# Performance work log

Measured on AMD Instinct MI355X. Metric: run time of the kernel, lower is better.

The kernel has to match this reference:

```python
import jax, jax.numpy as jnp
import numpy as np
import itertools

B, H, W, C = 64, 28, 28, 576
NH, WS = 18, 7
KD = C // NH          # head dim = 32 (attn_ratio=1 so d == key_dim)
HID = 4 * C           # mlp hidden
N = WS * WS           # tokens per window = 49


def _bias_idxs():
    points = list(itertools.product(range(WS), range(WS)))
    offsets, idxs = {}, []
    for p1 in points:
        for p2 in points:
            off = (abs(p1[0] - p2[0]), abs(p1[1] - p2[1]))
            if off not in offsets:
                offsets[off] = len(offsets)
            idxs.append(offsets[off])
    return np.asarray(idxs, dtype=np.int64).reshape(N, N), len(offsets)


def setup_inputs() -> dict:
    key = jax.random.key(0)
    ks = jax.random.split(key, 10)
    idxs, n_off = _bias_idxs()  # n_off == 49
    s = 0.02
    return {
        "x": jax.random.normal(ks[0], (B, H * W, C), jnp.float32),
        "gamma_a": jnp.ones((C,), jnp.float32),
        "beta_a": jnp.zeros((C,), jnp.float32),
        "qkv_w": jax.random.normal(ks[1], (3 * C, C), jnp.float32) * s,
        "qkv_b": jnp.zeros((3 * C,), jnp.float32),
        "proj_w": jax.random.normal(ks[2], (C, C), jnp.float32) * s,
        "proj_b": jnp.zeros((C,), jnp.float32),
        "attn_biases": jax.random.normal(ks[3], (NH, n_off), jnp.float32) * s,
        "conv_w": jax.random.normal(ks[4], (C, 1, 3, 3), jnp.float32) * 0.1,
        "bn_gamma": jnp.ones((C,), jnp.float32),
        "bn_beta": jnp.zeros((C,), jnp.float32),
        "bn_mean": jnp.zeros((C,), jnp.float32),
        "bn_var": jax.random.uniform(ks[5], (C,), jnp.float32, 0.5, 1.5),
        "gamma_m": jnp.ones((C,), jnp.float32),
        "beta_m": jnp.zeros((C,), jnp.float32),
        "fc1_w": jax.random.normal(ks[6], (HID, C), jnp.float32) * s,
        "fc1_b": jnp.zeros((HID,), jnp.float32),
        "fc2_w": jax.random.normal(ks[7], (C, HID), jnp.float32) * s,
        "fc2_b": jnp.zeros((C,), jnp.float32),
        "bias_idxs": jnp.asarray(idxs),
    }


def _ln(x, g, b, eps=1e-5):
    mu = x.mean(-1, keepdims=True)
    var = ((x - mu) ** 2).mean(-1, keepdims=True)
    return (x - mu) * jax.lax.rsqrt(var + eps) * g + b


def reference(x, gamma_a, beta_a, qkv_w, qkv_b, proj_w, proj_b, attn_biases,
              conv_w, bn_gamma, bn_beta, bn_mean, bn_var,
              gamma_m, beta_m, fc1_w, fc1_b, fc2_w, fc2_b, bias_idxs):
    scale = KD ** -0.5
    nWh, nWw = H // WS, W // WS
    res = x
    # ---- window partition: (B, H*W, C) -> (B*nWh*nWw, 49, C) ----
    xw = x.reshape(B, nWh, WS, nWw, WS, C).transpose(0, 1, 3, 2, 4, 5)
    xw = xw.reshape(-1, N, C)
    # ---- windowed attention with gathered relative-position bias ----
    h = _ln(xw, gamma_a, beta_a)
    qkv = h @ qkv_w.T + qkv_b                       # (Bw, N, 3C)
    qkv = qkv.reshape(-1, N, NH, 3 * KD)
    q, k, v = jnp.split(qkv, 3, axis=-1)            # each (Bw, N, NH, KD)
    q = q.transpose(0, 2, 1, 3)
    k = k.transpose(0, 2, 1, 3)
    v = v.transpose(0, 2, 1, 3)
    bias = attn_biases[:, bias_idxs]                # (NH, N, N)
    attn = jnp.einsum('bhnd,bhmd->bhnm', q, k) * scale + bias
    attn = jax.nn.softmax(attn, axis=-1)
    out = jnp.einsum('bhnm,bhmd->bhnd', attn, v)    # (Bw, NH, N, KD)
    out = out.transpose(0, 2, 1, 3).reshape(-1, N, C) @ proj_w.T + proj_b
    # ---- window reverse ----
    out = out.reshape(B, nWh, nWw, WS, WS, C).transpose(0, 1, 3, 2, 4, 5)
    out = out.reshape(B, H * W, C)
    x = res + out
    # ---- depthwise 3x3 conv + BatchNorm (inference stats) ----
    xc = x.transpose(0, 2, 1).reshape(B, C, H, W)
    xc = jax.lax.conv_general_dilated(
        xc, conv_w, (1, 1), [(1, 1), (1, 1)],
        feature_group_count=C,
        dimension_numbers=('NCHW', 'OIHW', 'NCHW'))
    eps = 1e-5
    inv = (jax.lax.rsqrt(bn_var + eps) * bn_gamma)[:, None, None]
    xc = (xc - bn_mean[:, None, None]) * inv + bn_beta[:, None, None]
    x = xc.reshape(B, C, H * W).transpose(0, 2, 1)
    # ---- MLP with pre-LayerNorm ----
    hm = _ln(x, gamma_m, beta_m)
    hm = jax.nn.gelu(hm @ fc1_w.T + fc1_b, approximate=False)
    hm = hm @ fc2_w.T + fc2_b
    return x + hm
```

## Files before the change

kernel.cpp:

```cpp
#include <hip/hip_runtime.h>
#include <hip/hip_bf16.h>

typedef __bf16 v8bf  __attribute__((ext_vector_type(8)));
typedef __bf16 v4bf  __attribute__((ext_vector_type(4)));
typedef float  f32x4 __attribute__((ext_vector_type(4)));
typedef float  f32x8 __attribute__((ext_vector_type(8)));

#define TOKENS 50176
#define CDIM   576
#define NHEAD  18
#define QKVD   1728

__device__ __forceinline__ void gld16(const __bf16* g, __bf16* l)
{
    __builtin_amdgcn_global_load_lds(
        (const __attribute__((address_space(1))) void*)g,
        (__attribute__((address_space(3))) void*)l,
        16, 0, 0);
}

__device__ __forceinline__ float fast_gelu(float x)
{
    const float z  = x * 0.70710678118654752f;
    const float az = fabsf(z);
    const float t  = __frcp_rn(1.0f + 0.3275911f * az);
    float p = 1.061405429f;
    p = p * t - 1.453152027f;
    p = p * t + 1.421413741f;
    p = p * t - 0.284496736f;
    p = p * t + 0.254829592f;
    const float e   = __expf(-z * z);
    float erfv = 1.0f - p * t * e;
    erfv = copysignf(erfv, z);
    return 0.5f * x * (1.0f + erfv);
}

__global__ __launch_bounds__(256)
void cast_kernel(const float* __restrict__ in, __bf16* __restrict__ out)
{
    const size_t i = ((size_t)blockIdx.x * 256 + threadIdx.x) * 4;
    f32x4 v = *(const f32x4*)&in[i];
    v4bf o;
#pragma unroll
    for (int j = 0; j < 4; ++j) o[j] = (__bf16)v[j];
    *(v4bf*)&out[i] = o;
}

__global__ __launch_bounds__(64)
void conv_prep(const float* __restrict__ w, const float* __restrict__ bg,
               const float* __restrict__ bb, const float* __restrict__ bm,
               const float* __restrict__ bv, __bf16* __restrict__ wt,
               float* __restrict__ bias2)
{
    const int c = blockIdx.x * 64 + threadIdx.x;
    const float inv = rsqrtf(bv[c] + 1e-5f) * bg[c];
#pragma unroll
    for (int t = 0; t < 9; ++t) wt[t * CDIM + c] = (__bf16)(w[c * 9 + t] * inv);
    bias2[c] = bb[c] - bm[c] * inv;
}

__global__ __launch_bounds__(256)
void ln_kernel(const float* __restrict__ x, const float* __restrict__ g,
               const float* __restrict__ b, __bf16* __restrict__ out)
{
    const int lane = threadIdx.x & 63;
    const int wid  = threadIdx.x >> 6;
    const size_t t = (size_t)blockIdx.x * 4 + wid;
    const float* row = x + t * CDIM;

    float v[16];
    float sum = 0.f, sq = 0.f;
    {
        f32x8 d0 = *(const f32x8*)&row[(size_t)lane * 8];
#pragma unroll
        for (int j = 0; j < 8; ++j) { float f = d0[j]; v[j] = f; sum += f; sq += f * f; }
    }
    if (lane < 8) {
        f32x8 d1 = *(const f32x8*)&row[(size_t)(lane + 64) * 8];
#pragma unroll
        for (int j = 0; j < 8; ++j) { float f = d1[j]; v[8 + j] = f; sum += f; sq += f * f; }
    }
#pragma unroll
    for (int o = 32; o >= 1; o >>= 1) {
        sum += __shfl_xor(sum, o, 64);
        sq  += __shfl_xor(sq,  o, 64);
    }
    const float mean = sum * (1.0f / CDIM);
    const float rstd = rsqrtf(sq * (1.0f / CDIM) - mean * mean + 1e-5f);

    {
        int c0 = lane * 8;
        v8bf o0;
#pragma unroll
        for (int j = 0; j < 8; ++j)
            o0[j] = (__bf16)((v[j] - mean) * rstd * g[c0 + j] + b[c0 + j]);
        *(v8bf*)&out[t * CDIM + c0] = o0;
    }
    if (lane < 8) {
        int c0 = (lane + 64) * 8;
        v8bf o1;
#pragma unroll
        for (int j = 0; j < 8; ++j)
            o1[j] = (__bf16)((v[8 + j] - mean) * rstd * g[c0 + j] + b[c0 + j]);
        *(v8bf*)&out[t * CDIM + c0] = o1;
    }
}

template<int BM, int EPI, typename OutT, typename AddT>
__global__ __launch_bounds__(512, 1)
void gemm_bt(const __bf16* __restrict__ A, const __bf16* __restrict__ W,
             const float* __restrict__ bias, const AddT* __restrict__ add,
             OutT* __restrict__ C, int N, int K, int nN)
{
    constexpr int BK  = 32;
    constexpr int ASZ = BM * BK;
    constexpr int BSZ = 192 * BK;
    constexpr int MFR = BM / 32;
    constexpr int MH  = MFR / 2;
    __shared__ __bf16 L[4][ASZ + BSZ];
    const int tid = threadIdx.x, lane = tid & 63, wid = tid >> 6;
    const int lr = lane & 15, kh = lane >> 4;
    const int wm = wid >> 2, wn = wid & 3;

    const int nwg = gridDim.x, bid = blockIdx.x;
    const int q = nwg >> 3, r = nwg & 7;
    const int xcd = bid & 7, jc = bid >> 3;
    const int wgid = (xcd < r ? xcd * (q + 1) : r * (q + 1) + (xcd - r) * q) + jc;
    const int mblk = wgid / nN, nblk = wgid - mblk * nN;
    const int m0 = mblk * BM, n0 = nblk * 192;

    const __bf16* pA;
    if constexpr (BM == 256) pA = A + (size_t)(m0 + wid * 32 + lr) * K + kh * 8;
    else                     pA = A + (size_t)(m0 + wid * 16 + lr) * K + kh * 8;
    const __bf16* pW = W + (size_t)(n0 + (wid < 6 ? wid : 0) * 32 + lr) * K + kh * 8;

    auto stageA = [&](int s, int kt) {
        if constexpr (BM == 256) {
#pragma unroll
            for (int i = 0; i < 2; ++i)
                gld16(pA + (size_t)(i * 16) * K + kt * BK, &L[s][(wid * 2 + i) * 512]);
        } else {
            gld16(pA + kt * BK, &L[s][wid * 512]);
        }
    };
    auto stageB = [&](int s, int kt) {
        if (wid < 6) {
#pragma unroll
            for (int i = 0; i < 2; ++i)
                gld16(pW + (size_t)(i * 16) * K + kt * BK,
                      &L[s][ASZ + (wid * 2 + i) * 512]);
        }
    };

    const int lo = lane * 8;

    f32x4 acc[MFR][3] = {};
    const int NT = K / BK;

    stageA(0, 0); stageB(0, 0);
    stageA(1, 1); stageB(1, 1);

    for (int t = 0; t < NT; ++t) {
        if (t + 1 < NT) {
            if constexpr (BM == 256) {
                if (wid < 6) asm volatile("s_waitcnt vmcnt(4)" ::: "memory");
                else         asm volatile("s_waitcnt vmcnt(2)" ::: "memory");
            } else {
                if (wid < 6) asm volatile("s_waitcnt vmcnt(3)" ::: "memory");
                else         asm volatile("s_waitcnt vmcnt(1)" ::: "memory");
            }
        } else {
            asm volatile("s_waitcnt vmcnt(0)" ::: "memory");
        }
        __builtin_amdgcn_s_barrier();

        const __bf16* Ls = L[t & 3];
        v8bf bfr[3], afr[MH];

#pragma unroll
        for (int nf = 0; nf < 3; ++nf)
            bfr[nf] = *(const v8bf*)&Ls[ASZ + (wn * 3 + nf) * 512 + lo];
#pragma unroll
        for (int mf = 0; mf < MH; ++mf)
            afr[mf] = *(const v8bf*)&Ls[(wm * MFR + mf) * 512 + lo];

        if (t + 2 < NT) stageA((t + 2) & 3, t + 2);

        __builtin_amdgcn_s_setprio(1);
#pragma unroll
        for (int mf = 0; mf < MH; ++mf)
#pragma unroll
            for (int nf = 0; nf < 3; ++nf)
                acc[mf][nf] = __builtin_amdgcn_mfma_f32_16x16x32_bf16(
                    afr[mf], bfr[nf], acc[mf][nf], 0, 0, 0);
        __builtin_amdgcn_s_setprio(0);
        __builtin_amdgcn_s_barrier();

#pragma unroll
        for (int mf = 0; mf < MH; ++mf)
            afr[mf] = *(const v8bf*)&Ls[(wm * MFR + MH + mf) * 512 + lo];

        if (t + 2 < NT) stageB((t + 2) & 3, t + 2);

        __builtin_amdgcn_s_setprio(1);
#pragma unroll
        for (int mf = 0; mf < MH; ++mf)
#pragma unroll
            for (int nf = 0; nf < 3; ++nf)
                acc[MH + mf][nf] = __builtin_amdgcn_mfma_f32_16x16x32_bf16(
                    afr[mf], bfr[nf], acc[MH + mf][nf], 0, 0, 0);
        __builtin_amdgcn_s_setprio(0);
    }

#pragma unroll
    for (int mf = 0; mf < MFR; ++mf)
#pragma unroll
        for (int nf = 0; nf < 3; ++nf)
#pragma unroll
            for (int rr = 0; rr < 4; ++rr) {
                int row = m0 + wm * (BM / 2) + mf * 16 + kh * 4 + rr;
                int col = n0 + wn * 48 + nf * 16 + lr;
                float vv = acc[mf][nf][rr] + bias[col];
                if (EPI == 1) vv += (float)add[(size_t)row * N + col];
                if (EPI == 2) vv = fast_gelu(vv);
                C[(size_t)row * N + col] = (OutT)vv;
            }
}

__global__ __launch_bounds__(64)
void attn_kernel(const __bf16* __restrict__ qkv, const float* __restrict__ biases,
                 const int* __restrict__ bidx, __bf16* __restrict__ out)
{
    const int head = blockIdx.x;
    const int win  = blockIdx.y;
    const int tid  = threadIdx.x;
    const int b  = win >> 4;
    const int wy = (win >> 2) & 3;
    const int wx = win & 3;
    __shared__ float kk[49][32];
    __shared__ float vv[49][32];
    const size_t hb = (size_t)head * 96;

    for (int e = tid; e < 49 * 32; e += 64) {
        int n = e >> 5, d = e & 31;
        int iy = n / 7, ix = n - iy * 7;
        size_t t = (size_t)b * 784 + (size_t)(wy * 7 + iy) * 28 + wx * 7 + ix;
        const __bf16* p = qkv + t * QKVD + hb;
        kk[n][d] = (float)p[32 + d];
        vv[n][d] = (float)p[64 + d];
    }
    float q[32];
    size_t tmine = 0;
    if (tid < 49) {
        int iy = tid / 7, ix = tid - iy * 7;
        tmine = (size_t)b * 784 + (size_t)(wy * 7 + iy) * 28 + wx * 7 + ix;
        const __bf16* p = qkv + tmine * QKVD + hb;
#pragma unroll
        for (int d = 0; d < 32; ++d) q[d] = (float)p[d];
    }
    __syncthreads();
    if (tid >= 49) return;

    const float scale = 0.17677669529663687f;
    float s[49];
    float mx = -1e30f;
    const int*   brow = bidx + tid * 49;
    const float* bh   = biases + head * 49;
#pragma unroll
    for (int m = 0; m < 49; ++m) {
        float dot = 0.f;
#pragma unroll
        for (int d = 0; d < 32; ++d) dot += q[d] * kk[m][d];
        float val = dot * scale + bh[brow[m]];
        s[m] = val;
        mx = fmaxf(mx, val);
    }
    float sum = 0.f;
#pragma unroll
    for (int m = 0; m < 49; ++m) { float e = __expf(s[m] - mx); s[m] = e; sum += e; }
    const float rs = 1.0f / sum;

    __bf16* op = out + tmine * CDIM + (size_t)head * 32;
#pragma unroll
    for (int d = 0; d < 32; ++d) {
        float a = 0.f;
#pragma unroll
        for (int m = 0; m < 49; ++m) a += s[m] * vv[m][d];
        op[d] = (__bf16)(a * rs);
    }
}

__global__ __launch_bounds__(256)
void conv_bn_ln(const __bf16* __restrict__ xin, const __bf16* __restrict__ wt,
                const float* __restrict__ bias2, const float* __restrict__ g,
                const float* __restrict__ b,
                __bf16* __restrict__ x3, __bf16* __restrict__ lnm)
{
    const int lane = threadIdx.x & 63;
    const int wid  = threadIdx.x >> 6;
    const size_t p = (size_t)blockIdx.x * 4 + wid;
    const int bimg = (int)(p / 784);
    const int pix  = (int)(p - (size_t)bimg * 784);
    const int y = pix / 28, xx = pix - y * 28;
    const size_t rowbase = (size_t)bimg * 784;

    float v[16];
    float sum = 0.f, sq = 0.f;

    {
        const int c0 = lane * 8;
        float a[8];
        f32x4 b0 = *(const f32x4*)&bias2[c0];
        f32x4 b1 = *(const f32x4*)&bias2[c0 + 4];
#pragma unroll
        for (int j = 0; j < 4; ++j) { a[j] = b0[j]; a[4 + j] = b1[j]; }
#pragma unroll
        for (int dy = 0; dy < 3; ++dy) {
            int ny = y + dy - 1;
            if (ny < 0 || ny >= 28) continue;
#pragma unroll
            for (int dx = 0; dx < 3; ++dx) {
                int nx = xx + dx - 1;
                if (nx < 0 || nx >= 28) continue;
                v8bf xv = *(const v8bf*)&xin[(rowbase + ny * 28 + nx) * CDIM + c0];
                v8bf wv = *(const v8bf*)&wt[(dy * 3 + dx) * CDIM + c0];
#pragma unroll
                for (int j = 0; j < 8; ++j) a[j] += (float)xv[j] * (float)wv[j];
            }
        }
#pragma unroll
        for (int j = 0; j < 8; ++j) { v[j] = a[j]; sum += a[j]; sq += a[j] * a[j]; }
    }
    if (lane < 8) {
        const int c0 = 512 + lane * 8;
        float a[8];
        f32x4 b0 = *(const f32x4*)&bias2[c0];
        f32x4 b1 = *(const f32x4*)&bias2[c0 + 4];
#pragma unroll
        for (int j = 0; j < 4; ++j) { a[j] = b0[j]; a[4 + j] = b1[j]; }
#pragma unroll
        for (int dy = 0; dy < 3; ++dy) {
            int ny = y + dy - 1;
            if (ny < 0 || ny >= 28) continue;
#pragma unroll
            for (int dx = 0; dx < 3; ++dx) {
                int nx = xx + dx - 1;
                if (nx < 0 || nx >= 28) continue;
                v8bf xv = *(const v8bf*)&xin[(rowbase + ny * 28 + nx) * CDIM + c0];
                v8bf wv = *(const v8bf*)&wt[(dy * 3 + dx) * CDIM + c0];
#pragma unroll
                for (int j = 0; j < 8; ++j) a[j] += (float)xv[j] * (float)wv[j];
            }
        }
#pragma unroll
        for (int j = 0; j < 8; ++j) { v[8 + j] = a[j]; sum += a[j]; sq += a[j] * a[j]; }
    }

#pragma unroll
    for (int o = 32; o >= 1; o >>= 1) {
        sum += __shfl_xor(sum, o, 64);
        sq  += __shfl_xor(sq,  o, 64);
    }
    const float mean = sum * (1.0f / CDIM);
    const float rstd = rsqrtf(sq * (1.0f / CDIM) - mean * mean + 1e-5f);

    {
        const int c0 = lane * 8;
        v8bf o3, ol;
#pragma unroll
        for (int j = 0; j < 8; ++j) {
            o3[j] = (__bf16)v[j];
            ol[j] = (__bf16)((v[j] - mean) * rstd * g[c0 + j] + b[c0 + j]);
        }
        *(v8bf*)&x3[p * CDIM + c0]  = o3;
        *(v8bf*)&lnm[p * CDIM + c0] = ol;
    }
    if (lane < 8) {
        const int c0 = 512 + lane * 8;
        v8bf o3, ol;
#pragma unroll
        for (int j = 0; j < 8; ++j) {
            o3[j] = (__bf16)v[8 + j];
            ol[j] = (__bf16)((v[8 + j] - mean) * rstd * g[c0 + j] + b[c0 + j]);
        }
        *(v8bf*)&x3[p * CDIM + c0]  = o3;
        *(v8bf*)&lnm[p * CDIM + c0] = ol;
    }
}

extern "C" void kernel_launch(void* const* d_in, const int* in_sizes, int n_in,
                              void* d_out, int out_size, void* d_ws, size_t ws_size,
                              hipStream_t stream)
{
    (void)in_sizes; (void)n_in; (void)out_size; (void)ws_size;
    const float* x          = (const float*)d_in[0];
    const float* gamma_a    = (const float*)d_in[1];
    const float* beta_a     = (const float*)d_in[2];
    const float* qkv_w      = (const float*)d_in[3];
    const float* qkv_b      = (const float*)d_in[4];
    const float* proj_w     = (const float*)d_in[5];
    const float* proj_b     = (const float*)d_in[6];
    const float* attn_bias  = (const float*)d_in[7];
    const float* conv_w     = (const float*)d_in[8];
    const float* bn_g       = (const float*)d_in[9];
    const float* bn_b       = (const float*)d_in[10];
    const float* bn_m       = (const float*)d_in[11];
    const float* bn_v       = (const float*)d_in[12];
    const float* gamma_m    = (const float*)d_in[13];
    const float* beta_m     = (const float*)d_in[14];
    const float* fc1_w      = (const float*)d_in[15];
    const float* fc1_b      = (const float*)d_in[16];
    const float* fc2_w      = (const float*)d_in[17];
    const float* fc2_b      = (const float*)d_in[18];
    const int*   bidx       = (const int*)d_in[19];

    const size_t T = TOKENS;
    __bf16* ws     = (__bf16*)d_ws;
    __bf16* hbuf   = ws;
    __bf16* qkvbuf = ws + T * 576;
    __bf16* aout   = ws;
    __bf16* x2     = ws + T * 2304;
    __bf16* x3     = ws + T * 2880;
    __bf16* lnm    = ws;
    __bf16* f1     = ws + T * 576;
    __bf16* wq     = x3 + T * 576;
    __bf16* wp     = wq + (size_t)QKVD * CDIM;
    __bf16* w1     = wp + (size_t)CDIM * CDIM;
    __bf16* w2     = w1 + (size_t)2304 * CDIM;
    __bf16* wt     = w2 + (size_t)CDIM * 2304;
    float*  bias2  = (float*)(wt + 9 * CDIM);
    float*  outp   = (float*)d_out;

    cast_kernel<<<dim3((QKVD * CDIM) / 1024), 256, 0, stream>>>(qkv_w, wq);
    cast_kernel<<<dim3((CDIM * CDIM) / 1024), 256, 0, stream>>>(proj_w, wp);
    cast_kernel<<<dim3((2304 * CDIM) / 1024), 256, 0, stream>>>(fc1_w, w1);
    cast_kernel<<<dim3((CDIM * 2304) / 1024), 256, 0, stream>>>(fc2_w, w2);
    conv_prep<<<dim3(9), 64, 0, stream>>>(conv_w, bn_g, bn_b, bn_m, bn_v, wt, bias2);

    ln_kernel<<<dim3(T / 4), 256, 0, stream>>>(x, gamma_a, beta_a, hbuf);
    gemm_bt<256, 0, __bf16, float><<<dim3(196 * 9), 512, 0, stream>>>(
        hbuf, wq, qkv_b, nullptr, qkvbuf, QKVD, CDIM, 9);
    attn_kernel<<<dim3(NHEAD, 1024), 64, 0, stream>>>(qkvbuf, attn_bias, bidx, aout);
    gemm_bt<128, 1, __bf16, float><<<dim3(392 * 3), 512, 0, stream>>>(
        aout, wp, proj_b, x, x2, CDIM, CDIM, 3);
    conv_bn_ln<<<dim3(12544), 256, 0, stream>>>(x2, wt, bias2, gamma_m, beta_m,
                                                x3, lnm);
    gemm_bt<256, 2, __bf16, float><<<dim3(196 * 12), 512, 0, stream>>>(
        lnm, w1, fc1_b, nullptr, f1, 2304, CDIM, 12);
    gemm_bt<128, 1, float, __bf16><<<dim3(392 * 3), 512, 0, stream>>>(
        f1, w2, fc2_b, x3, outp, CDIM, 2304, 3);
}
```

Baseline: 1.054 ms.

## Use 256-row GEMM tiles everywhere, vectorize attention, merge weight casts

All four GEMMs now use a single 256-row tile, so the proj and fc2 GEMMs launch half as many workgroups (588 instead of 1176), each doing twice the work with more weight reuse. The attention kernel loads Q/K/V with 16-byte vector loads and computes dot products and the weighted V sum with float4 vector arithmetic, replacing scalar bf16 loads and stores. The four weight-cast launches are merged into one kernel. Fewer workgroups on the N=576 GEMMs may cut occupancy across the device's compute units.

New measurement: 1.003 ms (median of 2 runs). 4.9% less time.

```diff
diff --git a/kernel.cpp b/kernel.cpp
--- a/kernel.cpp
+++ b/kernel.cpp
@@ -36,14 +36,24 @@
 }
 
 __global__ __launch_bounds__(256)
-void cast_kernel(const float* __restrict__ in, __bf16* __restrict__ out)
+void cast4_kernel(const float* __restrict__ s0, const float* __restrict__ s1,
+                  const float* __restrict__ s2, const float* __restrict__ s3,
+                  __bf16* __restrict__ dst)
 {
     const size_t i = ((size_t)blockIdx.x * 256 + threadIdx.x) * 4;
-    f32x4 v = *(const f32x4*)&in[i];
+    constexpr size_t n0 = (size_t)QKVD * CDIM;
+    constexpr size_t n1 = n0 + (size_t)CDIM * CDIM;
+    constexpr size_t n2 = n1 + (size_t)2304 * CDIM;
+    const float* s; size_t off;
+    if (i < n0)      { s = s0; off = i; }
+    else if (i < n1) { s = s1; off = i - n0; }
+    else if (i < n2) { s = s2; off = i - n1; }
+    else             { s = s3; off = i - n2; }
+    f32x4 v = *(const f32x4*)&s[off];
     v4bf o;
 #pragma unroll
     for (int j = 0; j < 4; ++j) o[j] = (__bf16)v[j];
-    *(v4bf*)&out[i] = o;
+    *(v4bf*)&dst[i] = o;
 }
 
 __global__ __launch_bounds__(64)
@@ -106,17 +116,15 @@
     }
 }
 
-template<int BM, int EPI, typename OutT, typename AddT>
+template<int EPI, typename OutT, typename AddT>
 __global__ __launch_bounds__(512, 1)
 void gemm_bt(const __bf16* __restrict__ A, const __bf16* __restrict__ W,
              const float* __restrict__ bias, const AddT* __restrict__ add,
              OutT* __restrict__ C, int N, int K, int nN)
 {
     constexpr int BK  = 32;
-    constexpr int ASZ = BM * BK;
+    constexpr int ASZ = 256 * BK;
     constexpr int BSZ = 192 * BK;
-    constexpr int MFR = BM / 32;
-    constexpr int MH  = MFR / 2;
     __shared__ __bf16 L[4][ASZ + BSZ];
     const int tid = threadIdx.x, lane = tid & 63, wid = tid >> 6;
     const int lr = lane & 15, kh = lane >> 4;
@@ -127,21 +135,15 @@
     const int xcd = bid & 7, jc = bid >> 3;
     const int wgid = (xcd < r ? xcd * (q + 1) : r * (q + 1) + (xcd - r) * q) + jc;
     const int mblk = wgid / nN, nblk = wgid - mblk * nN;
-    const int m0 = mblk * BM, n0 = nblk * 192;
-
-    const __bf16* pA;
-    if constexpr (BM == 256) pA = A + (size_t)(m0 + wid * 32 + lr) * K + kh * 8;
-    else                     pA = A + (size_t)(m0 + wid * 16 + lr) * K + kh * 8;
+    const int m0 = mblk * 256, n0 = nblk * 192;
+
+    const __bf16* pA = A + (size_t)(m0 + wid * 32 + lr) * K + kh * 8;
     const __bf16* pW = W + (size_t)(n0 + (wid < 6 ? wid : 0) * 32 + lr) * K + kh * 8;
 
     auto stageA = [&](int s, int kt) {
-        if constexpr (BM == 256) {
-#pragma unroll
-            for (int i = 0; i < 2; ++i)
-                gld16(pA + (size_t)(i * 16) * K + kt * BK, &L[s][(wid * 2 + i) * 512]);
-        } else {
-            gld16(pA + kt * BK, &L[s][wid * 512]);
-        }
+#pragma unroll
+        for (int i = 0; i < 2; ++i)
+            gld16(pA + (size_t)(i * 16) * K + kt * BK, &L[s][(wid * 2 + i) * 512]);
     };
     auto stageB = [&](int s, int kt) {
         if (wid < 6) {
@@ -154,7 +156,7 @@
 
     const int lo = lane * 8;
 
-    f32x4 acc[MFR][3] = {};
+    f32x4 acc[8][3] = {};
     const int NT = K / BK;
 
     stageA(0, 0); stageB(0, 0);
@@ -162,33 +164,28 @@
 
     for (int t = 0; t < NT; ++t) {
         if (t + 1 < NT) {
-            if constexpr (BM == 256) {
-                if (wid < 6) asm volatile("s_waitcnt vmcnt(4)" ::: "memory");
-                else         asm volatile("s_waitcnt vmcnt(2)" ::: "memory");
-            } else {
-                if (wid < 6) asm volatile("s_waitcnt vmcnt(3)" ::: "memory");
-                else         asm volatile("s_waitcnt vmcnt(1)" ::: "memory");
-            }
+            if (wid < 6) asm volatile("s_waitcnt vmcnt(4)" ::: "memory");
+            else         asm volatile("s_waitcnt vmcnt(2)" ::: "memory");
         } else {
             asm volatile("s_waitcnt vmcnt(0)" ::: "memory");
         }
         __builtin_amdgcn_s_barrier();
 
         const __bf16* Ls = L[t & 3];
-        v8bf bfr[3], afr[MH];
+        v8bf bfr[3], afr[4];
 
 #pragma unroll
         for (int nf = 0; nf < 3; ++nf)
             bfr[nf] = *(const v8bf*)&Ls[ASZ + (wn * 3 + nf) * 512 + lo];
 #pragma unroll
-        for (int mf = 0; mf < MH; ++mf)
-            afr[mf] = *(const v8bf*)&Ls[(wm * MFR + mf) * 512 + lo];
+        for (int mf = 0; mf < 4; ++mf)
+            afr[mf] = *(const v8bf*)&Ls[(wm * 8 + mf) * 512 + lo];
 
         if (t + 2 < NT) stageA((t + 2) & 3, t + 2);
 
         __builtin_amdgcn_s_setprio(1);
 #pragma unroll
-        for (int mf = 0; mf < MH; ++mf)
+        for (int mf = 0; mf < 4; ++mf)
 #pragma unroll
             for (int nf = 0; nf < 3; ++nf)
                 acc[mf][nf] = __builtin_amdgcn_mfma_f32_16x16x32_bf16(
@@ -197,28 +194,28 @@
         __builtin_amdgcn_s_barrier();
 
 #pragma unroll
-        for (int mf = 0; mf < MH; ++mf)
-            afr[mf] = *(const v8bf*)&Ls[(wm * MFR + MH + mf) * 512 + lo];
+        for (int mf = 0; mf < 4; ++mf)
+            afr[mf] = *(const v8bf*)&Ls[(wm * 8 + 4 + mf) * 512 + lo];
 
         if (t + 2 < NT) stageB((t + 2) & 3, t + 2);
 
         __builtin_amdgcn_s_setprio(1);
 #pragma unroll
-        for (int mf = 0; mf < MH; ++mf)
+        for (int mf = 0; mf < 4; ++mf)
 #pragma unroll
             for (int nf = 0; nf < 3; ++nf)
-                acc[MH + mf][nf] = __builtin_amdgcn_mfma_f32_16x16x32_bf16(
-                    afr[mf], bfr[nf], acc[MH + mf][nf], 0, 0, 0);
+                acc[4 + mf][nf] = __builtin_amdgcn_mfma_f32_16x16x32_bf16(
+                    afr[mf], bfr[nf], acc[4 + mf][nf], 0, 0, 0);
         __builtin_amdgcn_s_setprio(0);
     }
 
 #pragma unroll
-    for (int mf = 0; mf < MFR; ++mf)
+    for (int mf = 0; mf < 8; ++mf)
 #pragma unroll
         for (int nf = 0; nf < 3; ++nf)
 #pragma unroll
             for (int rr = 0; rr < 4; ++rr) {
-                int row = m0 + wm * (BM / 2) + mf * 16 + kh * 4 + rr;
+                int row = m0 + wm * 128 + mf * 16 + kh * 4 + rr;
                 int col = n0 + wn * 48 + nf * 16 + lr;
                 float vv = acc[mf][nf][rr] + bias[col];
                 if (EPI == 1) vv += (float)add[(size_t)row * N + col];
@@ -241,22 +238,39 @@
     __shared__ float vv[49][32];
     const size_t hb = (size_t)head * 96;
 
-    for (int e = tid; e < 49 * 32; e += 64) {
-        int n = e >> 5, d = e & 31;
-        int iy = n / 7, ix = n - iy * 7;
-        size_t t = (size_t)b * 784 + (size_t)(wy * 7 + iy) * 28 + wx * 7 + ix;
+    for (int e = tid; e < 196; e += 64) {
+        const int n = e >> 2, j = e & 3;
+        const int iy = n / 7, ix = n - iy * 7;
+        const size_t t = (size_t)b * 784 + (size_t)(wy * 7 + iy) * 28 + wx * 7 + ix;
         const __bf16* p = qkv + t * QKVD + hb;
-        kk[n][d] = (float)p[32 + d];
-        vv[n][d] = (float)p[64 + d];
-    }
-    float q[32];
+        v8bf k8 = *(const v8bf*)&p[32 + j * 8];
+        v8bf v8 = *(const v8bf*)&p[64 + j * 8];
+        f32x4 k0, k1, v0, v1;
+#pragma unroll
+        for (int r = 0; r < 4; ++r) {
+            k0[r] = (float)k8[r]; k1[r] = (float)k8[4 + r];
+            v0[r] = (float)v8[r]; v1[r] = (float)v8[4 + r];
+        }
+        *(f32x4*)&kk[n][j * 8]     = k0;
+        *(f32x4*)&kk[n][j * 8 + 4] = k1;
+        *(f32x4*)&vv[n][j * 8]     = v0;
+        *(f32x4*)&vv[n][j * 8 + 4] = v1;
+    }
+    f32x4 qv[8];
     size_t tmine = 0;
     if (tid < 49) {
-        int iy = tid / 7, ix = tid - iy * 7;
+        const int iy = tid / 7, ix = tid - iy * 7;
         tmine = (size_t)b * 784 + (size_t)(wy * 7 + iy) * 28 + wx * 7 + ix;
         const __bf16* p = qkv + tmine * QKVD + hb;
 #pragma unroll
-        for (int d = 0; d < 32; ++d) q[d] = (float)p[d];
+        for (int jj = 0; jj < 4; ++jj) {
+            v8bf q8 = *(const v8bf*)&p[jj * 8];
+#pragma unroll
+            for (int r = 0; r < 4; ++r) {
+                qv[2 * jj][r]     = (float)q8[r];
+                qv[2 * jj + 1][r] = (float)q8[4 + r];
+            }
+        }
     }
     __syncthreads();
     if (tid >= 49) return;
@@ -268,10 +282,11 @@
     const float* bh   = biases + head * 49;
 #pragma unroll
     for (int m = 0; m < 49; ++m) {
-        float dot = 0.f;
-#pragma unroll
-        for (int d = 0; d < 32; ++d) dot += q[d] * kk[m][d];
-        float val = dot * scale + bh[brow[m]];
+        const f32x4* krow = (const f32x4*)&kk[m][0];
+        f32x4 d4 = {0.f, 0.f, 0.f, 0.f};
+#pragma unroll
+        for (int j = 0; j < 8; ++j) d4 += qv[j] * krow[j];
+        float val = (d4[0] + d4[1] + d4[2] + d4[3]) * scale + bh[brow[m]];
         s[m] = val;
         mx = fmaxf(mx, val);
     }
@@ -280,13 +295,25 @@
     for (int m = 0; m < 49; ++m) { float e = __expf(s[m] - mx); s[m] = e; sum += e; }
     const float rs = 1.0f / sum;
 
+    f32x4 av[8] = {};
+#pragma unroll
+    for (int m = 0; m < 49; ++m) {
+        const float sm = s[m];
+        const f32x4* vrow = (const f32x4*)&vv[m][0];
+#pragma unroll
+        for (int j = 0; j < 8; ++j) av[j] += sm * vrow[j];
+    }
+
     __bf16* op = out + tmine * CDIM + (size_t)head * 32;
 #pragma unroll
-    for (int d = 0; d < 32; ++d) {
-        float a = 0.f;
-#pragma unroll
-        for (int m = 0; m < 49; ++m) a += s[m] * vv[m][d];
-        op[d] = (__bf16)(a * rs);
+    for (int jj = 0; jj < 4; ++jj) {
+        v8bf o;
+#pragma unroll
+        for (int r = 0; r < 4; ++r) {
+            o[r]     = (__bf16)(av[2 * jj][r] * rs);
+            o[4 + r] = (__bf16)(av[2 * jj + 1][r] * rs);
+        }
+        *(v8bf*)&op[jj * 8] = o;
     }
 }
 
@@ -431,22 +458,19 @@
     float*  bias2  = (float*)(wt + 9 * CDIM);
     float*  outp   = (float*)d_out;
 
-    cast_kernel<<<dim3((QKVD * CDIM) / 1024), 256, 0, stream>>>(qkv_w, wq);
-    cast_kernel<<<dim3((CDIM * CDIM) / 1024), 256, 0, stream>>>(proj_w, wp);
-    cast_kernel<<<dim3((2304 * CDIM) / 1024), 256, 0, stream>>>(fc1_w, w1);
-    cast_kernel<<<dim3((CDIM * 2304) / 1024), 256, 0, stream>>>(fc2_w, w2);
+    cast4_kernel<<<dim3(3888), 256, 0, stream>>>(qkv_w, proj_w, fc1_w, fc2_w, wq);
     conv_prep<<<dim3(9), 64, 0, stream>>>(conv_w, bn_g, bn_b, bn_m, bn_v, wt, bias2);
 
     ln_kernel<<<dim3(T / 4), 256, 0, stream>>>(x, gamma_a, beta_a, hbuf);
-    gemm_bt<256, 0, __bf16, float><<<dim3(196 * 9), 512, 0, stream>>>(
+    gemm_bt<0, __bf16, float><<<dim3(196 * 9), 512, 0, stream>>>(
         hbuf, wq, qkv_b, nullptr, qkvbuf, QKVD, CDIM, 9);
     attn_kernel<<<dim3(NHEAD, 1024), 64, 0, stream>>>(qkvbuf, attn_bias, bidx, aout);
-    gemm_bt<128, 1, __bf16, float><<<dim3(392 * 3), 512, 0, stream>>>(
+    gemm_bt<1, __bf16, float><<<dim3(196 * 3), 512, 0, stream>>>(
         aout, wp, proj_b, x, x2, CDIM, CDIM, 3);
     conv_bn_ln<<<dim3(12544), 256, 0, stream>>>(x2, wt, bias2, gamma_m, beta_m,
                                                 x3, lnm);
-    gemm_bt<256, 2, __bf16, float><<<dim3(196 * 12), 512, 0, stream>>>(
+    gemm_bt<2, __bf16, float><<<dim3(196 * 12), 512, 0, stream>>>(
         lnm, w1, fc1_b, nullptr, f1, 2304, CDIM, 12);
-    gemm_bt<128, 1, float, __bf16><<<dim3(392 * 3), 512, 0, stream>>>(
+    gemm_bt<1, float, __bf16><<<dim3(196 * 3), 512, 0, stream>>>(
         f1, w2, fc2_b, x3, outp, CDIM, 2304, 3);
 }
```
